# Kernel tuning notes

Measured on AMD Instinct MI355X. Metric: run time of the kernel, lower is better.

Reference implementation:

```python
import jax, jax.numpy as jnp
import numpy as np

N_NODES = 50000
N_EDGES = 800000
IN_DIM = 128
HID_DIM = 128
OUT_DIM = 128


def setup_inputs() -> dict:
    key = jax.random.key(0)
    k = jax.random.split(key, 8)
    x = jax.random.normal(k[0], (N_NODES, IN_DIM), dtype=jnp.float32)
    edge_index = jax.random.randint(k[1], (2, N_EDGES), 0, N_NODES, dtype=jnp.int64)
    edge_weight = jax.random.uniform(k[2], (N_EDGES,), dtype=jnp.float32)
    # GCNConv params: weight [in, out] (glorot-ish), bias [out]
    W1 = jax.random.normal(k[3], (IN_DIM, HID_DIM), dtype=jnp.float32) / np.sqrt(IN_DIM)
    b1 = jnp.zeros((HID_DIM,), dtype=jnp.float32)
    W2 = jax.random.normal(k[4], (HID_DIM, OUT_DIM), dtype=jnp.float32) / np.sqrt(HID_DIM)
    b2 = jnp.zeros((OUT_DIM,), dtype=jnp.float32)
    return {"x": x, "edge_index": edge_index, "edge_weight": edge_weight,
            "W1": W1, "b1": b1, "W2": W2, "b2": b2}


def gcn_conv(x, W, b, src, dst, ew, n_nodes):
    """PyG GCNConv: add self-loops (weight 1), symmetric D^-1/2 (A+I) D^-1/2 norm."""
    h = x @ W  # [N, out]
    deg = jax.ops.segment_sum(ew, dst, num_segments=n_nodes) + 1.0  # +1 for self loop
    dis = jnp.where(deg > 0, jax.lax.rsqrt(deg), 0.0)  # deg^{-1/2}
    norm = dis[src] * ew * dis[dst]  # [E]
    msg = h[src] * norm[:, None]  # gather + weight -> [E, out]
    agg = jax.ops.segment_sum(msg, dst, num_segments=n_nodes)
    # self-loop contribution: norm_ii = dis[i] * 1 * dis[i]
    agg = agg + h * (dis * dis)[:, None]
    return agg + b


def reference(x, edge_index, edge_weight, W1, b1, W2, b2):
    src, dst = edge_index[0], edge_index[1]
    n = x.shape[0]
    h = gcn_conv(x, W1, b1, src, dst, edge_weight, n)
    h = jax.nn.relu(h)
    out = gcn_conv(h, W2, b2, src, dst, edge_weight, n)
    return out
```

## Files before the change

kernel.cpp:

```cpp
#include <hip/hip_runtime.h>

#define NDIM 128

typedef __attribute__((ext_vector_type(8))) short bf16x8;
typedef __attribute__((ext_vector_type(4))) float floatx4;

__device__ __forceinline__ float bflo(unsigned v){ return __uint_as_float(v << 16); }
__device__ __forceinline__ float bfhi(unsigned v){ return __uint_as_float(v & 0xffff0000u); }
__device__ __forceinline__ unsigned f2bf(float f){
  unsigned u = __float_as_uint(f);
  return (u + 0x7fffu + ((u >> 16) & 1u)) >> 16;
}

__global__ void k_prep0(unsigned long long* __restrict__ pk,
                        const float* __restrict__ W1, const float* __restrict__ W2,
                        unsigned short* __restrict__ Wp1, unsigned short* __restrict__ Wp2,
                        int n){
  int i = blockIdx.x * 256 + threadIdx.x;
  if (i < n) pk[i] = 0ULL;
  if (i < NDIM * NDIM){
    int k = i >> 7, c = i & 127;
    int kt = k >> 5, kq = (k >> 3) & 3, j = k & 7;
    int Lb = kq * 16 + (c & 15);
    int idx = (((kt * 8 + (c >> 4)) * 64) + Lb) * 8 + j;
    Wp1[idx] = (unsigned short)f2bf(W1[i]);
    Wp2[idx] = (unsigned short)f2bf(W2[i]);
  }
}

__global__ void k_deg(const int* __restrict__ ei, const float* __restrict__ ew,
                      unsigned long long* pk, int E){
  int e = blockIdx.x * blockDim.x + threadIdx.x;
  if (e >= E) return;
  int d = ei[E + e];
  unsigned fx = (unsigned)__float2uint_rn(ew[e] * 1048576.0f);
  atomicAdd(&pk[d], (1ULL << 44) | (unsigned long long)fx);
}

__global__ __launch_bounds__(1024) void k_scan1(const unsigned long long* __restrict__ pk,
                                                int* __restrict__ off,
                                                int* __restrict__ bsum, int n){
  __shared__ int wsum[16];
  int t = threadIdx.x;
  int i = blockIdx.x * 1024 + t;
  int c = (i < n) ? (int)(pk[i] >> 44) : 0;
  int lane = t & 63, w = t >> 6;
  int v = c;
  #pragma unroll
  for (int d = 1; d < 64; d <<= 1){ int u = __shfl_up(v, d); if (lane >= d) v += u; }
  if (lane == 63) wsum[w] = v;
  __syncthreads();
  if (w == 0){
    int sv = (lane < 16) ? wsum[lane] : 0;
    #pragma unroll
    for (int d = 1; d < 16; d <<= 1){ int u = __shfl_up(sv, d); if (lane >= d) sv += u; }
    if (lane < 16) wsum[lane] = sv;
  }
  __syncthreads();
  int base = (w > 0) ? wsum[w - 1] : 0;
  if (i < n) off[i] = base + v - c;
  if (t == 1023) bsum[blockIdx.x] = wsum[15];
}

__global__ __launch_bounds__(1024) void k_scan23(int* __restrict__ off, int* __restrict__ cur,
                                                 const int* __restrict__ bsum,
                                                 const unsigned long long* __restrict__ pk,
                                                 float* __restrict__ dis, int n, int E, int nb){
  __shared__ int sBase;
  int t = threadIdx.x;
  if (t < 64){
    int c2 = (t < nb) ? bsum[t] : 0;
    int v2 = c2;
    #pragma unroll
    for (int d = 1; d < 64; d <<= 1){ int u = __shfl_up(v2, d); if (t >= d) v2 += u; }
    if (t == (int)blockIdx.x) sBase = v2 - c2;
  }
  __syncthreads();
  int i = blockIdx.x * 1024 + t;
  if (i == 0) off[n] = E;
  if (i >= n) return;
  int o = off[i] + sBase;
  off[i] = o; cur[i] = o;
  float deg = 1.0f + (float)(pk[i] & ((1ULL << 44) - 1)) * (1.0f / 1048576.0f);
  dis[i] = rsqrtf(deg);
}

__global__ void k_place(const int* __restrict__ ei, const float* __restrict__ ew,
                        const float* __restrict__ dis, int* cur, unsigned* edges, int E){
  int e = blockIdx.x * blockDim.x + threadIdx.x;
  if (e >= E) return;
  int s = ei[e], d = ei[E + e];
  int p = atomicAdd(&cur[d], 1);
  edges[p] = (f2bf(dis[s] * ew[e] * dis[d]) << 16) | (unsigned)s;
}

template<int XF32>
__global__ __launch_bounds__(256) void k_gemm_mfma(const void* __restrict__ Xv,
                                                   const unsigned short* __restrict__ Wp,
                                                   unsigned short* __restrict__ Hout,
                                                   int ntiles){
  __shared__ unsigned short Wb[4 * 8 * 64 * 8];
  int tid = threadIdx.x;
  for (int t = tid; t < 2048; t += 256)
    ((uint4*)Wb)[t] = ((const uint4*)Wp)[t];
  __syncthreads();

  int w = tid >> 6, L = tid & 63;
  int m = L & 15, q = L >> 4;
  for (int tile = blockIdx.x * 4 + w; tile < ntiles; tile += gridDim.x * 4){
    size_t row = (size_t)tile * 16 + m;
    floatx4 acc[8] = {};
    #pragma unroll
    for (int kt = 0; kt < 4; ++kt){
      bf16x8 a;
      if (XF32){
        const float* xp = (const float*)Xv + row * NDIM + kt * 32 + q * 8;
        float4 a0 = *(const float4*)xp;
        float4 a1 = *(const float4*)(xp + 4);
        unsigned short* as = (unsigned short*)&a;
        as[0] = f2bf(a0.x); as[1] = f2bf(a0.y); as[2] = f2bf(a0.z); as[3] = f2bf(a0.w);
        as[4] = f2bf(a1.x); as[5] = f2bf(a1.y); as[6] = f2bf(a1.z); as[7] = f2bf(a1.w);
      } else {
        a = *(const bf16x8*)((const unsigned short*)Xv + row * NDIM + kt * 32 + q * 8);
      }
      #pragma unroll
      for (int ct = 0; ct < 8; ++ct){
        bf16x8 b = *(const bf16x8*)&Wb[((kt * 8 + ct) * 64 + L) * 8];
        acc[ct] = __builtin_amdgcn_mfma_f32_16x16x32_bf16(a, b, acc[ct], 0, 0, 0);
      }
    }
    #pragma unroll
    for (int ct = 0; ct < 8; ++ct){
      #pragma unroll
      for (int r = 0; r < 4; ++r){
        size_t orow = (size_t)tile * 16 + q * 4 + r;
        Hout[orow * NDIM + ct * 16 + m] = (unsigned short)f2bf(acc[ct][r]);
      }
    }
  }
}

template<int OUT_F32>
__global__ __launch_bounds__(256) void k_agg(const unsigned short* __restrict__ H,
                                             const int* __restrict__ off,
                                             const unsigned* __restrict__ edges,
                                             const float* __restrict__ dis,
                                             const float* __restrict__ bias,
                                             void* __restrict__ out,
                                             int n, int do_relu){
  int g = threadIdx.x >> 6, L = threadIdx.x & 63;
  int i = blockIdx.x * 4 + g;
  if (i >= n) return;
  float di = dis[i];
  float dii = di * di;
  float2 bv = ((const float2*)bias)[L];
  unsigned hv = ((const unsigned*)(H + (size_t)i * NDIM))[L];
  float acc0 = fmaf(bflo(hv), dii, bv.x);
  float acc1 = fmaf(bfhi(hv), dii, bv.y);
  int p  = __builtin_amdgcn_readfirstlane(off[i]);
  int p1 = __builtin_amdgcn_readfirstlane(off[i + 1]);
  const char* Hb = (const char*)H;
  unsigned L4 = (unsigned)L * 4u;

  while (p + 16 <= p1){
    unsigned e[16], h[16];
    #pragma unroll
    for (int j = 0; j < 16; ++j) e[j] = __builtin_amdgcn_readfirstlane(edges[p + j]);
    #pragma unroll
    for (int j = 0; j < 16; ++j)
      h[j] = *(const unsigned*)(Hb + (((size_t)(e[j] & 0xFFFFu)) << 8) + L4);
    #pragma unroll
    for (int j = 0; j < 16; ++j){
      float w = bfhi(e[j]);
      acc0 = fmaf(bflo(h[j]), w, acc0);
      acc1 = fmaf(bfhi(h[j]), w, acc1);
    }
    p += 16;
  }
  while (p + 4 <= p1){
    unsigned e[4], h[4];
    #pragma unroll
    for (int j = 0; j < 4; ++j) e[j] = __builtin_amdgcn_readfirstlane(edges[p + j]);
    #pragma unroll
    for (int j = 0; j < 4; ++j)
      h[j] = *(const unsigned*)(Hb + (((size_t)(e[j] & 0xFFFFu)) << 8) + L4);
    #pragma unroll
    for (int j = 0; j < 4; ++j){
      float w = bfhi(e[j]);
      acc0 = fmaf(bflo(h[j]), w, acc0);
      acc1 = fmaf(bfhi(h[j]), w, acc1);
    }
    p += 4;
  }
  for (; p < p1; ++p){
    unsigned e = __builtin_amdgcn_readfirstlane(edges[p]);
    unsigned h2 = *(const unsigned*)(Hb + (((size_t)(e & 0xFFFFu)) << 8) + L4);
    float w = bfhi(e);
    acc0 = fmaf(bflo(h2), w, acc0);
    acc1 = fmaf(bfhi(h2), w, acc1);
  }
  if (do_relu){ acc0 = fmaxf(acc0, 0.f); acc1 = fmaxf(acc1, 0.f); }
  if (OUT_F32){
    ((float2*)((float*)out + (size_t)i * NDIM))[L] = make_float2(acc0, acc1);
  } else {
    ((unsigned*)((unsigned short*)out + (size_t)i * NDIM))[L] = (f2bf(acc1) << 16) | f2bf(acc0);
  }
}

extern "C" void kernel_launch(void* const* d_in, const int* in_sizes, int n_in,
                              void* d_out, int out_size, void* d_ws, size_t ws_size,
                              hipStream_t stream){
  const float* x  = (const float*)d_in[0];
  const int*   ei = (const int*)  d_in[1];
  const float* ew = (const float*)d_in[2];
  const float* W1 = (const float*)d_in[3];
  const float* b1 = (const float*)d_in[4];
  const float* W2 = (const float*)d_in[5];
  const float* b2 = (const float*)d_in[6];
  float* out = (float*)d_out;
  int N = in_sizes[0] / NDIM;
  int E = in_sizes[2];
  int nb = (N + 1023) / 1024;
  int ntiles = N / 16;

  char* p = (char*)d_ws;
  auto alloc = [&](size_t b) -> char* { char* r = p; p += (b + 255) & ~(size_t)255; return r; };
  unsigned long long* pk = (unsigned long long*)alloc((size_t)N * 8);
  float*    dis   = (float*)   alloc((size_t)N * 4);
  int*      cur   = (int*)     alloc((size_t)N * 4);
  int*      off   = (int*)     alloc((size_t)(N + 1) * 4);
  int*      bsum  = (int*)     alloc((size_t)64 * 4);
  unsigned short* Wp1 = (unsigned short*)alloc(NDIM * NDIM * 2);
  unsigned short* Wp2 = (unsigned short*)alloc(NDIM * NDIM * 2);
  unsigned* edges = (unsigned*)alloc((size_t)E * 4);
  unsigned short* R = (unsigned short*)alloc((size_t)N * NDIM * 2);
  unsigned short* H1 = (unsigned short*)d_out;

  k_prep0<<<(N + 255) / 256, 256, 0, stream>>>(pk, W1, W2, Wp1, Wp2, N);
  k_deg  <<<(E + 255) / 256, 256, 0, stream>>>(ei, ew, pk, E);
  k_scan1<<<nb, 1024, 0, stream>>>(pk, off, bsum, N);
  k_scan23<<<nb, 1024, 0, stream>>>(off, cur, bsum, pk, dis, N, E, nb);
  k_place<<<(E + 255) / 256, 256, 0, stream>>>(ei, ew, dis, cur, edges, E);

  int gg = (ntiles + 3) / 4;
  k_gemm_mfma<1><<<gg, 256, 0, stream>>>(x, Wp1, H1, ntiles);
  k_agg<0> <<<(N + 3) / 4, 256, 0, stream>>>(H1, off, edges, dis, b1, R, N, 1);
  k_gemm_mfma<0><<<gg, 256, 0, stream>>>(R, Wp2, R, ntiles);
  k_agg<1> <<<(N + 3) / 4, 256, 0, stream>>>(R, off, edges, dis, b2, out, N, 0);
}
```

Baseline: 249.6 us.

## Precompute per-edge rank in degree pass and partition CSR placement by destination range

The degree atomic now returns the previous count, which is stored as a per-edge rank. Placement then computes each edge's slot directly as off[d]+rank instead of taking a second atomic on a cursor array. Placement is also split into 8 destination-range partitions, each scanning a chunk of edges, so that writes from a block land in a narrower address range for cache locality. In exchange, each partition rereads the dst index array for every edge (8x the reads), a rank array is added, and the 16-bit rank assumes no node has more than 65535 incoming edges.

```diff
diff --git a/kernel.cpp b/kernel.cpp
--- a/kernel.cpp
+++ b/kernel.cpp
@@ -1,6 +1,7 @@
 #include <hip/hip_runtime.h>
 
 #define NDIM 128
+#define NPART 8
 
 typedef __attribute__((ext_vector_type(8))) short bf16x8;
 typedef __attribute__((ext_vector_type(4))) float floatx4;
@@ -29,12 +30,13 @@
 }
 
 __global__ void k_deg(const int* __restrict__ ei, const float* __restrict__ ew,
-                      unsigned long long* pk, int E){
+                      unsigned long long* pk, unsigned short* __restrict__ rank, int E){
   int e = blockIdx.x * blockDim.x + threadIdx.x;
   if (e >= E) return;
   int d = ei[E + e];
   unsigned fx = (unsigned)__float2uint_rn(ew[e] * 1048576.0f);
-  atomicAdd(&pk[d], (1ULL << 44) | (unsigned long long)fx);
+  unsigned long long old = atomicAdd(&pk[d], (1ULL << 44) | (unsigned long long)fx);
+  rank[e] = (unsigned short)(old >> 44);
 }
 
 __global__ __launch_bounds__(1024) void k_scan1(const unsigned long long* __restrict__ pk,
@@ -62,7 +64,7 @@
   if (t == 1023) bsum[blockIdx.x] = wsum[15];
 }
 
-__global__ __launch_bounds__(1024) void k_scan23(int* __restrict__ off, int* __restrict__ cur,
+__global__ __launch_bounds__(1024) void k_scan23(int* __restrict__ off,
                                                  const int* __restrict__ bsum,
                                                  const unsigned long long* __restrict__ pk,
                                                  float* __restrict__ dis, int n, int E, int nb){
@@ -79,19 +81,34 @@
   int i = blockIdx.x * 1024 + t;
   if (i == 0) off[n] = E;
   if (i >= n) return;
-  int o = off[i] + sBase;
-  off[i] = o; cur[i] = o;
+  off[i] += sBase;
   float deg = 1.0f + (float)(pk[i] & ((1ULL << 44) - 1)) * (1.0f / 1048576.0f);
   dis[i] = rsqrtf(deg);
 }
 
-__global__ void k_place(const int* __restrict__ ei, const float* __restrict__ ew,
-                        const float* __restrict__ dis, int* cur, unsigned* edges, int E){
-  int e = blockIdx.x * blockDim.x + threadIdx.x;
-  if (e >= E) return;
-  int s = ei[e], d = ei[E + e];
-  int p = atomicAdd(&cur[d], 1);
-  edges[p] = (f2bf(dis[s] * ew[e] * dis[d]) << 16) | (unsigned)s;
+__global__ __launch_bounds__(256) void k_place(const int* __restrict__ ei,
+                                               const float* __restrict__ ew,
+                                               const unsigned short* __restrict__ rank,
+                                               const float* __restrict__ dis,
+                                               const int* __restrict__ off,
+                                               unsigned* __restrict__ edges,
+                                               int E, int N){
+  int pid = blockIdx.x % NPART;
+  int cid = blockIdx.x / NPART;
+  int C   = gridDim.x / NPART;
+  int per = (E + C - 1) / C;
+  int e0 = cid * per;
+  int e1 = min(e0 + per, E);
+  int lo = (int)(((long long)pid * N) / NPART);
+  int hi = (int)(((long long)(pid + 1) * N) / NPART);
+  for (int e = e0 + threadIdx.x; e < e1; e += 256){
+    int d = ei[E + e];
+    if (d < lo || d >= hi) continue;
+    int s = ei[e];
+    float w = ew[e];
+    int p = off[d] + (int)rank[e];
+    edges[p] = (f2bf(dis[s] * w * dis[d]) << 16) | (unsigned)s;
+  }
 }
 
 template<int XF32>
@@ -227,9 +244,9 @@
   auto alloc = [&](size_t b) -> char* { char* r = p; p += (b + 255) & ~(size_t)255; return r; };
   unsigned long long* pk = (unsigned long long*)alloc((size_t)N * 8);
   float*    dis   = (float*)   alloc((size_t)N * 4);
-  int*      cur   = (int*)     alloc((size_t)N * 4);
   int*      off   = (int*)     alloc((size_t)(N + 1) * 4);
   int*      bsum  = (int*)     alloc((size_t)64 * 4);
+  unsigned short* rank = (unsigned short*)alloc((size_t)E * 2);
   unsigned short* Wp1 = (unsigned short*)alloc(NDIM * NDIM * 2);
   unsigned short* Wp2 = (unsigned short*)alloc(NDIM * NDIM * 2);
   unsigned* edges = (unsigned*)alloc((size_t)E * 4);
@@ -237,10 +254,10 @@
   unsigned short* H1 = (unsigned short*)d_out;
 
   k_prep0<<<(N + 255) / 256, 256, 0, stream>>>(pk, W1, W2, Wp1, Wp2, N);
-  k_deg  <<<(E + 255) / 256, 256, 0, stream>>>(ei, ew, pk, E);
+  k_deg  <<<(E + 255) / 256, 256, 0, stream>>>(ei, ew, pk, rank, E);
   k_scan1<<<nb, 1024, 0, stream>>>(pk, off, bsum, N);
-  k_scan23<<<nb, 1024, 0, stream>>>(off, cur, bsum, pk, dis, N, E, nb);
-  k_place<<<(E + 255) / 256, 256, 0, stream>>>(ei, ew, dis, cur, edges, E);
+  k_scan23<<<nb, 1024, 0, stream>>>(off, bsum, pk, dis, N, E, nb);
+  k_place<<<NPART * 96, 256, 0, stream>>>(ei, ew, rank, dis, off, edges, E, N);
 
   int gg = (ntiles + 3) / 4;
   k_gemm_mfma<1><<<gg, 256, 0, stream>>>(x, Wp1, H1, ntiles);
```

Result: faster. 238.5 us (-4.5%).
